# Kernel tuning notes

Hardware: AMD Instinct MI355X
Metric: run time of the kernel (lower is better)

Reference implementation:

```python
import jax, jax.numpy as jnp
import numpy as np

B, S, D = 8, 2048, 256


def setup_inputs() -> dict:
    key = jax.random.key(0)
    ks = jax.random.split(key, 8)
    nodes = jax.random.normal(ks[0], (B, S, D), dtype=jnp.float32)
    mask = jax.random.randint(ks[1], (B, S), 0, 2, dtype=jnp.int32)
    # ensure at least one unmasked position per row to avoid all--inf softmax
    mask = mask.at[:, 0].set(1)
    scale = 1.0 / np.sqrt(D)
    Wq = jax.random.normal(ks[2], (D, D), dtype=jnp.float32) * scale
    bq = jnp.zeros((D,), dtype=jnp.float32)
    Wk = jax.random.normal(ks[3], (D, D), dtype=jnp.float32) * scale
    bk = jnp.zeros((D,), dtype=jnp.float32)
    Wv = jax.random.normal(ks[4], (D, D), dtype=jnp.float32) * scale
    bv = jnp.zeros((D,), dtype=jnp.float32)
    return {"nodes": nodes, "mask": mask, "Wq": Wq, "bq": bq,
            "Wk": Wk, "bk": bk, "Wv": Wv, "bv": bv}


def reference(nodes, mask, Wq, bq, Wk, bk, Wv, bv):
    # Linear layers: x @ W.T + b (torch nn.Linear convention)
    q = jnp.einsum('bsd,ed->bse', nodes, Wq) + bq   # [B,S,D]
    k = jnp.einsum('bsd,ed->bse', nodes, Wk) + bk
    v = jnp.einsum('bsd,ed->bse', nodes, Wv) + bv
    d = k.shape[-1]
    scores = jnp.einsum('bqd,bkd->bqk', q, k) / jnp.sqrt(jnp.float32(d))  # [B,S,S]
    # mask[b, j] == 0 masks key column j for every query row
    scores = jnp.where(mask[:, None, :] != 0, scores, -jnp.inf)
    attn = jax.nn.softmax(scores, axis=-1)           # [B,S,S]
    weighted = jnp.einsum('bqk,bkd->bqd', attn, v)   # [B,S,D]
    return jnp.mean(weighted, axis=1)                # [B,D]
```

## Files before the change

kernel.cpp:

```cpp
#include <hip/hip_runtime.h>
#include <hip/hip_bf16.h>
#include <stdint.h>


typedef short short8 __attribute__((ext_vector_type(8)));
typedef float floatx4 __attribute__((ext_vector_type(4)));

#define MFMA16(a, b, c) __builtin_amdgcn_mfma_f32_16x16x32_bf16((a), (b), (c), 0, 0, 0)

#define ASYNC16(gsrc, ldst)                                                    \
    __builtin_amdgcn_global_load_lds(                                          \
        (__attribute__((address_space(1))) void*)(void*)(gsrc),                \
        (__attribute__((address_space(3))) void*)(ldst), 16, 0, 0)

static __device__ __forceinline__ unsigned short f2bf(float f) {
    union { float f; unsigned u; } v; v.f = f;
    unsigned r = v.u + 0x7fffu + ((v.u >> 16) & 1u);
    return (unsigned short)(r >> 16);
}

__global__ __launch_bounds__(256) void k_cc(
    const float* __restrict__ nodes, const float* __restrict__ Wq,
    const float* __restrict__ Wk, const float* __restrict__ Wv,
    unsigned short* __restrict__ nbf, unsigned short* __restrict__ wbf,
    const int* __restrict__ mask, int* __restrict__ cnt,
    int* __restrict__ slot_of ,
    unsigned short* __restrict__ kbt, unsigned short* __restrict__ vbt,
    float* __restrict__ outp )
{
    int blk = blockIdx.x;
    if (blk < 2144) {
        int unit = blk * 256 + threadIdx.x;
        const float* src;
        unsigned short* dst;
        int off;
        if (unit < 524288) {
            src = nodes; dst = nbf; off = unit * 8;
        } else {
            int j = (unit - 524288) * 8;
            int m = j >> 16;
            int r = j & 65535;
            src = (m == 0) ? Wq : (m == 1 ? Wk : Wv);
            dst = wbf + m * 65536;
            off = r;
        }
        float4 a = *(const float4*)(src + off);
        float4 b = *(const float4*)(src + off + 4);
        short8 o;
        o[0] = f2bf(a.x); o[1] = f2bf(a.y); o[2] = f2bf(a.z); o[3] = f2bf(a.w);
        o[4] = f2bf(b.x); o[5] = f2bf(b.y); o[6] = f2bf(b.z); o[7] = f2bf(b.w);
        *(short8*)(dst + off) = o;
        return;
    }
    if (blk < 2152) {
        if (threadIdx.x < 64) {
            int b = blk - 2144, lane = threadIdx.x;
            int base = 0;
            for (int c = 0; c < 2048; c += 64) {
                int m = mask[b * 2048 + c + lane];
                unsigned long long bal = __ballot(m != 0);
                int pre = __popcll(bal & ((1ull << lane) - 1ull));
                slot_of[b * 2048 + c + lane] = m ? (base + pre) : -1;
                base += __popcll(bal);
            }
            if (lane == 0) cnt[b] = base;
            int cntPad = (base + 63) & ~63;
            int pad = cntPad - base;
            short8 z8 = {};
            for (int i = lane; i < pad * 32; i += 64) {
                int slot = base + (i >> 5);
                int du = i & 31;
                size_t off = ((size_t)b * 32 + (slot >> 6)) * 16384
                           + ((size_t)du * 64 + (slot & 63)) * 8;
                *(short8*)(kbt + off) = z8;
            }
            for (int i = lane; i < pad * 256; i += 64) {
                int s = base + (i >> 8);
                int d = i & 255;
                int byte = ((d * 64 + (s & 63)) * 2) ^ ((d & 7) << 4);
                vbt[((size_t)b * 32 + (s >> 6)) * 16384 + (byte >> 1)] = 0;
            }
        }
        return;
    }
    int idx = (blk - 2152) * 256 + threadIdx.x;
    float4 z = {0.f, 0.f, 0.f, 0.f};
    if (idx < 512) ((float4*)outp)[idx] = z;
}

__global__ __launch_bounds__(256) void k_proj2b(
    const unsigned short* __restrict__ nbf,
    const unsigned short* __restrict__ wbf,
    const float* __restrict__ bq, const float* __restrict__ bk,
    const float* __restrict__ bv,
    const int* __restrict__ slot_of,
    unsigned short* __restrict__ qb, unsigned short* __restrict__ kbt,
    unsigned short* __restrict__ vbt)
{
    __shared__ __align__(16) unsigned short As[128 * 64];
    __shared__ __align__(16) unsigned short Bs[128 * 64];
    int tid = threadIdx.x, lane = tid & 63, wave = tid >> 6;
    int wm = wave & 1, wn = wave >> 1;
    int l15 = lane & 15, quad = lane >> 4;
    int mBase = blockIdx.x * 128;
    int nBase = blockIdx.y * 128;
    int z = blockIdx.z;
    const unsigned short* W = wbf + z * 65536;

    floatx4 acc[4][4] = {};

    for (int kc = 0; kc < 256; kc += 64) {
#pragma unroll
        for (int i = 0; i < 4; ++i) {
            int p = i * 256 + wave * 64 + lane;
            int row = p >> 3;
            int col8 = (p & 7) ^ (row & 7);
            int goff = row * 256 + kc + col8 * 8;
            unsigned short* dstA = &As[(i * 256 + wave * 64) * 8];
            unsigned short* dstB = &Bs[(i * 256 + wave * 64) * 8];
            ASYNC16(nbf + mBase * 256 + goff, dstA);
            ASYNC16(W + nBase * 256 + goff, dstB);
        }
        __syncthreads();
#pragma unroll
        for (int ks = 0; ks < 2; ++ks) {
            int c8 = ks * 4 + quad;
            short8 af[4], bfr[4];
#pragma unroll
            for (int i = 0; i < 4; ++i) {
                int row = wm * 64 + i * 16 + l15;
                af[i] = *(const short8*)(&As[(row * 8 + (c8 ^ (row & 7))) * 8]);
            }
#pragma unroll
            for (int i = 0; i < 4; ++i) {
                int row = wn * 64 + i * 16 + l15;
                bfr[i] = *(const short8*)(&Bs[(row * 8 + (c8 ^ (row & 7))) * 8]);
            }
#pragma unroll
            for (int mi = 0; mi < 4; ++mi)
#pragma unroll
                for (int ni = 0; ni < 4; ++ni)
                    acc[mi][ni] = MFMA16(af[mi], bfr[ni], acc[mi][ni]);
        }
        __syncthreads();
    }

    const float* bias = (z == 0) ? bq : (z == 1 ? bk : bv);
    if (z == 1) {
#pragma unroll
        for (int mi = 0; mi < 4; ++mi)
#pragma unroll
            for (int ni = 0; ni < 4; ++ni) {
                int col = nBase + wn * 64 + ni * 16 + l15;
                float bval = bias[col];
                int du = col >> 3, cj = col & 7;
#pragma unroll
                for (int r = 0; r < 4; ++r) {
                    int row = mBase + wm * 64 + mi * 16 + quad * 4 + r;
                    int slot = slot_of[row];
                    if (slot >= 0) {
                        int b = row >> 11;
                        size_t off = ((size_t)b * 32 + (slot >> 6)) * 16384
                                   + ((size_t)du * 64 + (slot & 63)) * 8 + cj;
                        kbt[off] = f2bf(acc[mi][ni][r] + bval);
                    }
                }
            }
    } else if (z == 2) {
#pragma unroll
        for (int mi = 0; mi < 4; ++mi)
#pragma unroll
            for (int ni = 0; ni < 4; ++ni) {
                int col = nBase + wn * 64 + ni * 16 + l15;
                float bval = bias[col];
#pragma unroll
                for (int r = 0; r < 4; ++r) {
                    int row = mBase + wm * 64 + mi * 16 + quad * 4 + r;
                    int slot = slot_of[row];
                    if (slot >= 0) {
                        int b = row >> 11;
                        int byte = ((col * 64 + (slot & 63)) * 2) ^ ((col & 7) << 4);
                        vbt[((size_t)b * 32 + (slot >> 6)) * 16384 + (byte >> 1)] =
                            f2bf(acc[mi][ni][r] + bval);
                    }
                }
            }
    } else {
        float scale = 0.0625f;
#pragma unroll
        for (int mi = 0; mi < 4; ++mi)
#pragma unroll
            for (int ni = 0; ni < 4; ++ni) {
                int col = nBase + wn * 64 + ni * 16 + l15;
                float bval = bias[col];
#pragma unroll
                for (int r = 0; r < 4; ++r) {
                    int row = mBase + wm * 64 + mi * 16 + quad * 4 + r;
                    qb[row * 256 + col] = f2bf((acc[mi][ni][r] + bval) * scale);
                }
            }
    }
}

__global__ __launch_bounds__(256, 1) void k_attn(
    const unsigned short* __restrict__ qb, const unsigned short* __restrict__ kbt,
    const unsigned short* __restrict__ vbt, const int* __restrict__ cnt_g,
    float* __restrict__ outp)
{
    __shared__ __align__(16) unsigned short kt[2][16384];
    __shared__ __align__(16) unsigned short vt[2][16384];
    __shared__ __align__(16) unsigned short pls[4][1024];
    __shared__ float l_s[4][16];
    int tid = threadIdx.x, lane = tid & 63, wave = tid >> 6;
    int l15 = lane & 15, quad = lane >> 4;
    int b = blockIdx.y;
    int cnt = cnt_g[b];
    int nchunk = (cnt + 63) >> 6;
    int qBase = blockIdx.x * 64 + wave * 16;

    short8 qf[8];
#pragma unroll
    for (int ks = 0; ks < 8; ++ks)
        qf[ks] = *(const short8*)(qb + (b * 2048 + qBase + l15) * 256 + ks * 32 + quad * 8);

    {
        const unsigned short* ksrc = kbt + ((size_t)b * 32) * 16384;
        const unsigned short* vsrc = vbt + ((size_t)b * 32) * 16384;
#pragma unroll
        for (int i = 0; i < 8; ++i) {
            int seg = wave * 8 + i;
            ASYNC16(ksrc + seg * 512 + lane * 8, &kt[0][seg * 512]);
            ASYNC16(vsrc + seg * 512 + lane * 8, &vt[0][seg * 512]);
        }
    }

    float ls[4] = {};
    floatx4 acco[4][4] = {};
    int p = 0;
    for (int c = 0; c < nchunk; ++c, p ^= 1) {
        if (c + 1 < nchunk) {
            const unsigned short* ksrc = kbt + ((size_t)b * 32 + c + 1) * 16384;
            const unsigned short* vsrc = vbt + ((size_t)b * 32 + c + 1) * 16384;
#pragma unroll
            for (int i = 0; i < 8; ++i) {
                int seg = wave * 8 + i;
                ASYNC16(ksrc + seg * 512 + lane * 8, &kt[p ^ 1][seg * 512]);
                ASYNC16(vsrc + seg * 512 + lane * 8, &vt[p ^ 1][seg * 512]);
            }
            asm volatile("s_waitcnt vmcnt(16)" ::: "memory");
        } else {
            asm volatile("s_waitcnt vmcnt(0)" ::: "memory");
        }
        __builtin_amdgcn_s_barrier();

        floatx4 sacc[4] = {};
#pragma unroll
        for (int ks = 0; ks < 8; ++ks)
#pragma unroll
            for (int nt = 0; nt < 4; ++nt) {
                short8 kf = *(const short8*)(&kt[p][((ks * 4 + quad) * 64 + nt * 16 + l15) * 8]);
                sacc[nt] = MFMA16(qf[ks], kf, sacc[nt]);
            }
#pragma unroll
        for (int nt = 0; nt < 4; ++nt) {
            float biasv = (c * 64 + nt * 16 + l15 < cnt) ? 0.0f : -1e30f;
#pragma unroll
            for (int r = 0; r < 4; ++r) {
                float e = __expf(sacc[nt][r] + biasv);
                ls[r] += e;
                int ql = quad * 4 + r;
                int byte = ((ql * 64 + nt * 16 + l15) * 2) ^ ((ql & 7) << 4);
                pls[wave][byte >> 1] = f2bf(e);
            }
        }
        asm volatile("s_waitcnt lgkmcnt(0)" ::: "memory");
        __builtin_amdgcn_sched_barrier(0);
        __builtin_amdgcn_s_barrier();

#pragma unroll
        for (int kr = 0; kr < 2; ++kr) {
            int pbyte = ((l15 * 64 + kr * 32 + quad * 8) * 2) ^ ((l15 & 7) << 4);
#pragma unroll
            for (int qt = 0; qt < 4; ++qt) {
                short8 pf = *(const short8*)(&pls[qt][pbyte >> 1]);
#pragma unroll
                for (int dtl = 0; dtl < 4; ++dtl) {
                    int dg = wave * 4 + dtl;
                    int vbyte = (((dg * 16 + l15) * 64 + kr * 32 + quad * 8) * 2)
                              ^ ((l15 & 7) << 4);
                    short8 vf = *(const short8*)((const char*)vt[p] + vbyte);
                    acco[qt][dtl] = MFMA16(vf, pf, acco[qt][dtl]);
                }
            }
        }
        __builtin_amdgcn_s_barrier();
    }

#pragma unroll
    for (int r = 0; r < 4; ++r) {
        float v = ls[r];
        v += __shfl_xor(v, 1); v += __shfl_xor(v, 2);
        v += __shfl_xor(v, 4); v += __shfl_xor(v, 8);
        ls[r] = v;
    }
    if (l15 == 0)
#pragma unroll
        for (int r = 0; r < 4; ++r) l_s[wave][quad * 4 + r] = ls[r];
    __syncthreads();

    float linv[4];
#pragma unroll
    for (int qt = 0; qt < 4; ++qt) linv[qt] = 1.0f / l_s[qt][l15];

#pragma unroll
    for (int dtl = 0; dtl < 4; ++dtl)
#pragma unroll
        for (int r = 0; r < 4; ++r) {
            float v = acco[0][dtl][r] * linv[0] + acco[1][dtl][r] * linv[1]
                    + acco[2][dtl][r] * linv[2] + acco[3][dtl][r] * linv[3];
            v += __shfl_xor(v, 1); v += __shfl_xor(v, 2);
            v += __shfl_xor(v, 4); v += __shfl_xor(v, 8);
            if (l15 == 0) {
                int d = (wave * 4 + dtl) * 16 + quad * 4 + r;
                atomicAdd(&outp[b * 256 + d], v * (1.0f / 2048.0f));
            }
        }
}

extern "C" void kernel_launch(void* const* d_in, const int* in_sizes, int n_in,
                              void* d_out, int out_size, void* d_ws, size_t ws_size,
                              hipStream_t stream)
{
    const float* nodes = (const float*)d_in[0];
    const int*   mask  = (const int*)d_in[1];
    const float* Wq    = (const float*)d_in[2];
    const float* bq    = (const float*)d_in[3];
    const float* Wk    = (const float*)d_in[4];
    const float* bk    = (const float*)d_in[5];
    const float* Wv    = (const float*)d_in[6];
    const float* bv    = (const float*)d_in[7];
    float* out = (float*)d_out;

    unsigned short* qb  = (unsigned short*)d_ws;
    unsigned short* vbt = qb + 4194304;
    int*   cnt  = (int*)(vbt + 4194304);
    int*   slot_of = cnt + 16;
    unsigned short* kbt = (unsigned short*)(slot_of + 16384);
    unsigned short* nbf = kbt + 4194304;
    unsigned short* wbf = nbf + 4194304;

    k_cc<<<2154, 256, 0, stream>>>(nodes, Wq, Wk, Wv, nbf, wbf,
                                   mask, cnt, slot_of, kbt, vbt, out);
    k_proj2b<<<dim3(128, 2, 3), 256, 0, stream>>>(nbf, wbf, bq, bk, bv,
                                                  slot_of, qb, kbt, vbt);
    k_attn<<<dim3(32, 8), 256, 0, stream>>>(qb, kbt, vbt, cnt, out);
}
```

Before: 149.8 us.

## Split attention block into 32-query tiles, read V directly from global

The attention kernel now processes 32 queries per block instead of 64. The four waves split the key columns of each chunk two ways for the score computation. V is no longer staged in LDS and is read straight from global or L2 in an unswizzled layout, and the projection and padding code write V in that plain layout. Launch bounds allow two blocks per CU and the grid doubles to 512 blocks. This raises occupancy and cuts LDS use, at the cost of V being reloaded from global memory by every block, with more redundant traffic and higher latency on the PV MFMAs.

```diff
diff --git a/kernel.cpp b/kernel.cpp
--- a/kernel.cpp
+++ b/kernel.cpp
@@ -77,8 +77,7 @@
             for (int i = lane; i < pad * 256; i += 64) {
                 int s = base + (i >> 8);
                 int d = i & 255;
-                int byte = ((d * 64 + (s & 63)) * 2) ^ ((d & 7) << 4);
-                vbt[((size_t)b * 32 + (s >> 6)) * 16384 + (byte >> 1)] = 0;
+                vbt[((size_t)b * 32 + (s >> 6)) * 16384 + d * 64 + (s & 63)] = 0;
             }
         }
         return;
@@ -179,9 +178,8 @@
                     int slot = slot_of[row];
                     if (slot >= 0) {
                         int b = row >> 11;
-                        int byte = ((col * 64 + (slot & 63)) * 2) ^ ((col & 7) << 4);
-                        vbt[((size_t)b * 32 + (slot >> 6)) * 16384 + (byte >> 1)] =
-                            f2bf(acc[mi][ni][r] + bval);
+                        vbt[((size_t)b * 32 + (slot >> 6)) * 16384
+                            + col * 64 + (slot & 63)] = f2bf(acc[mi][ni][r] + bval);
                     }
                 }
             }
@@ -202,21 +200,21 @@
     }
 }
 
-__global__ __launch_bounds__(256, 1) void k_attn(
+__global__ __launch_bounds__(256, 2) void k_attn(
     const unsigned short* __restrict__ qb, const unsigned short* __restrict__ kbt,
     const unsigned short* __restrict__ vbt, const int* __restrict__ cnt_g,
     float* __restrict__ outp)
 {
     __shared__ __align__(16) unsigned short kt[2][16384];
-    __shared__ __align__(16) unsigned short vt[2][16384];
-    __shared__ __align__(16) unsigned short pls[4][1024];
-    __shared__ float l_s[4][16];
+    __shared__ __align__(16) unsigned short pls[2][1024];
+    __shared__ float l_s[2][2][16];
     int tid = threadIdx.x, lane = tid & 63, wave = tid >> 6;
     int l15 = lane & 15, quad = lane >> 4;
-    int b = blockIdx.y;
+    int qh = wave & 1, kh = wave >> 1;
+    int b = blockIdx.x;
     int cnt = cnt_g[b];
     int nchunk = (cnt + 63) >> 6;
-    int qBase = blockIdx.x * 64 + wave * 16;
+    int qBase = blockIdx.y * 32 + qh * 16;
 
     short8 qf[8];
 #pragma unroll
@@ -225,75 +223,70 @@
 
     {
         const unsigned short* ksrc = kbt + ((size_t)b * 32) * 16384;
-        const unsigned short* vsrc = vbt + ((size_t)b * 32) * 16384;
 #pragma unroll
         for (int i = 0; i < 8; ++i) {
             int seg = wave * 8 + i;
             ASYNC16(ksrc + seg * 512 + lane * 8, &kt[0][seg * 512]);
-            ASYNC16(vsrc + seg * 512 + lane * 8, &vt[0][seg * 512]);
         }
     }
 
     float ls[4] = {};
-    floatx4 acco[4][4] = {};
+    floatx4 acco[2][4] = {};
     int p = 0;
     for (int c = 0; c < nchunk; ++c, p ^= 1) {
         if (c + 1 < nchunk) {
             const unsigned short* ksrc = kbt + ((size_t)b * 32 + c + 1) * 16384;
-            const unsigned short* vsrc = vbt + ((size_t)b * 32 + c + 1) * 16384;
 #pragma unroll
             for (int i = 0; i < 8; ++i) {
                 int seg = wave * 8 + i;
                 ASYNC16(ksrc + seg * 512 + lane * 8, &kt[p ^ 1][seg * 512]);
-                ASYNC16(vsrc + seg * 512 + lane * 8, &vt[p ^ 1][seg * 512]);
-            }
-            asm volatile("s_waitcnt vmcnt(16)" ::: "memory");
+            }
+            asm volatile("s_waitcnt vmcnt(8)" ::: "memory");
         } else {
             asm volatile("s_waitcnt vmcnt(0)" ::: "memory");
         }
         __builtin_amdgcn_s_barrier();
 
-        floatx4 sacc[4] = {};
+        floatx4 sacc[2] = {};
 #pragma unroll
         for (int ks = 0; ks < 8; ++ks)
 #pragma unroll
-            for (int nt = 0; nt < 4; ++nt) {
+            for (int j = 0; j < 2; ++j) {
+                int nt = kh * 2 + j;
                 short8 kf = *(const short8*)(&kt[p][((ks * 4 + quad) * 64 + nt * 16 + l15) * 8]);
-                sacc[nt] = MFMA16(qf[ks], kf, sacc[nt]);
-            }
-#pragma unroll
-        for (int nt = 0; nt < 4; ++nt) {
+                sacc[j] = MFMA16(qf[ks], kf, sacc[j]);
+            }
+#pragma unroll
+        for (int j = 0; j < 2; ++j) {
+            int nt = kh * 2 + j;
             float biasv = (c * 64 + nt * 16 + l15 < cnt) ? 0.0f : -1e30f;
 #pragma unroll
             for (int r = 0; r < 4; ++r) {
-                float e = __expf(sacc[nt][r] + biasv);
+                float e = __expf(sacc[j][r] + biasv);
                 ls[r] += e;
                 int ql = quad * 4 + r;
                 int byte = ((ql * 64 + nt * 16 + l15) * 2) ^ ((ql & 7) << 4);
-                pls[wave][byte >> 1] = f2bf(e);
+                *(unsigned short*)((char*)pls[qh] + byte) = f2bf(e);
             }
         }
         asm volatile("s_waitcnt lgkmcnt(0)" ::: "memory");
         __builtin_amdgcn_sched_barrier(0);
         __builtin_amdgcn_s_barrier();
 
+        const unsigned short* vsrc = vbt + ((size_t)b * 32 + c) * 16384;
 #pragma unroll
         for (int kr = 0; kr < 2; ++kr) {
             int pbyte = ((l15 * 64 + kr * 32 + quad * 8) * 2) ^ ((l15 & 7) << 4);
-#pragma unroll
-            for (int qt = 0; qt < 4; ++qt) {
-                short8 pf = *(const short8*)(&pls[qt][pbyte >> 1]);
-#pragma unroll
-                for (int dtl = 0; dtl < 4; ++dtl) {
-                    int dg = wave * 4 + dtl;
-                    int vbyte = (((dg * 16 + l15) * 64 + kr * 32 + quad * 8) * 2)
-                              ^ ((l15 & 7) << 4);
-                    short8 vf = *(const short8*)((const char*)vt[p] + vbyte);
-                    acco[qt][dtl] = MFMA16(vf, pf, acco[qt][dtl]);
-                }
-            }
-        }
-        __builtin_amdgcn_s_barrier();
+            short8 pf0 = *(const short8*)((const char*)pls[0] + pbyte);
+            short8 pf1 = *(const short8*)((const char*)pls[1] + pbyte);
+#pragma unroll
+            for (int dtl = 0; dtl < 4; ++dtl) {
+                int dg = wave * 4 + dtl;
+                short8 vf = *(const short8*)(vsrc + (dg * 16 + l15) * 64 + kr * 32 + quad * 8);
+                acco[0][dtl] = MFMA16(vf, pf0, acco[0][dtl]);
+                acco[1][dtl] = MFMA16(vf, pf1, acco[1][dtl]);
+            }
+        }
     }
 
 #pragma unroll
@@ -305,23 +298,23 @@
     }
     if (l15 == 0)
 #pragma unroll
-        for (int r = 0; r < 4; ++r) l_s[wave][quad * 4 + r] = ls[r];
+        for (int r = 0; r < 4; ++r) l_s[qh][kh][quad * 4 + r] = ls[r];
     __syncthreads();
 
-    float linv[4];
-#pragma unroll
-    for (int qt = 0; qt < 4; ++qt) linv[qt] = 1.0f / l_s[qt][l15];
+    float linv[2];
+#pragma unroll
+    for (int qt = 0; qt < 2; ++qt)
+        linv[qt] = 1.0f / (l_s[qt][0][l15] + l_s[qt][1][l15]);
 
 #pragma unroll
     for (int dtl = 0; dtl < 4; ++dtl)
 #pragma unroll
         for (int r = 0; r < 4; ++r) {
-            float v = acco[0][dtl][r] * linv[0] + acco[1][dtl][r] * linv[1]
-                    + acco[2][dtl][r] * linv[2] + acco[3][dtl][r] * linv[3];
+            float v = acco[0][dtl][r] * linv[0] + acco[1][dtl][r] * linv[1];
             v += __shfl_xor(v, 1); v += __shfl_xor(v, 2);
             v += __shfl_xor(v, 4); v += __shfl_xor(v, 8);
             if (l15 == 0) {
-                int d = (wave * 4 + dtl) * 16 + quad * 4 + r;
+                int d = wave * 64 + dtl * 16 + quad * 4 + r;
                 atomicAdd(&outp[b * 256 + d], v * (1.0f / 2048.0f));
             }
         }
@@ -353,5 +346,5 @@
                                    mask, cnt, slot_of, kbt, vbt, out);
     k_proj2b<<<dim3(128, 2, 3), 256, 0, stream>>>(nbf, wbf, bq, bk, bv,
                                                   slot_of, qb, kbt, vbt);
-    k_attn<<<dim3(32, 8), 256, 0, stream>>>(qb, kbt, vbt, cnt, out);
-}
+    k_attn<<<dim3(8, 64), 256, 0, stream>>>(qb, kbt, vbt, cnt, out);
+}
```

After: 168.0 us. +12.2%, slower.
